# Kernel optimization log

Hardware: AMD Instinct MI355X
Metric: run time of the kernel (lower is better)

## Reference

```python
import jax, jax.numpy as jnp
import numpy as np

B, L, H, NL = 2048, 32, 512, 64  # batch rows, max children, w_dim, num_labels
EPS = 1e-5


def _layernorm(x, g, b):
    mu = jnp.mean(x, axis=-1, keepdims=True)
    var = jnp.mean((x - mu) ** 2, axis=-1, keepdims=True)
    return (x - mu) * jax.lax.rsqrt(var + EPS) * g + b


def _lstm(x, Wih, Whh, bih, bhh):
    # x: [B, L, D] -> h: [B, L, H]; PyTorch gate order i, f, g, o
    Bs, Ls, _ = x.shape
    Hh = Whh.shape[1]
    xg = jnp.einsum('bld,gd->blg', x, Wih) + bih + bhh  # [B, L, 4H]

    def step(carry, xg_t):
        h, c = carry
        gates = xg_t + h @ Whh.T
        i, f, g, o = jnp.split(gates, 4, axis=-1)
        c = jax.nn.sigmoid(f) * c + jax.nn.sigmoid(i) * jnp.tanh(g)
        h = jax.nn.sigmoid(o) * jnp.tanh(c)
        return (h, c), h

    init = (jnp.zeros((Bs, Hh), x.dtype), jnp.zeros((Bs, Hh), x.dtype))
    _, hs = jax.lax.scan(step, init, jnp.swapaxes(xg, 0, 1))
    return jnp.swapaxes(hs, 0, 1)


def setup_inputs() -> dict:
    key = jax.random.key(0)
    ks = jax.random.split(key, 20)
    n = lambda k, shape, s=0.05: (jax.random.normal(k, shape, jnp.float32) * s)
    return {
        'children': n(ks[0], (B, L, H), 1.0),
        'ch_lengths': jax.random.randint(ks[1], (B,), 1, L + 1),
        'nt': n(ks[2], (B, H), 1.0),
        'nt_id': jax.random.randint(ks[3], (B,), 0, NL),
        'stack_state': n(ks[4], (B, H), 1.0),
        'Wih_f': n(ks[5], (4 * H, H)), 'Whh_f': n(ks[6], (4 * H, H)),
        'bih_f': jnp.zeros(4 * H, jnp.float32), 'bhh_f': jnp.zeros(4 * H, jnp.float32),
        'Wih_b': n(ks[7], (4 * H, H)), 'Whh_b': n(ks[8], (4 * H, H)),
        'bih_b': jnp.zeros(4 * H, jnp.float32), 'bhh_b': jnp.zeros(4 * H, jnp.float32),
        'V': n(ks[9], (2 * H, 2 * H)),
        'nt_emb': n(ks[10], (NL, H), 1.0),
        'nt_emb2': n(ks[11], (NL, 2 * H), 1.0),
        'ln1_g': jnp.ones(2 * H, jnp.float32), 'ln1_b': jnp.zeros(2 * H, jnp.float32),
        'ln2_g': jnp.ones(2 * H, jnp.float32), 'ln2_b': jnp.zeros(2 * H, jnp.float32),
        'gate_W': n(ks[12], (2 * H, 4 * H)), 'gate_b': jnp.zeros(2 * H, jnp.float32),
        'out_W': n(ks[13], (H, 2 * H)), 'out_b': jnp.zeros(H, jnp.float32),
    }


def reference(children, ch_lengths, nt, nt_id, stack_state,
              Wih_f, Whh_f, bih_f, bhh_f, Wih_b, Whh_b, bih_b, bhh_b,
              V, nt_emb, nt_emb2, ln1_g, ln1_b, ln2_g, ln2_b,
              gate_W, gate_b, out_W, out_b):
    t = jnp.arange(L)
    valid = (t[None, :] < ch_lengths[:, None])  # [B, L]
    mask = valid[:, :, None].astype(children.dtype)

    # forward direction (padded positions cannot affect earlier outputs)
    h_f = _lstm(children, Wih_f, Whh_f, bih_f, bhh_f) * mask

    # backward direction: emulate packed sequence by per-row reversal over true length
    rev_idx = jnp.clip(ch_lengths[:, None] - 1 - t[None, :], 0, L - 1)  # [B, L]
    x_rev = jnp.take_along_axis(children, rev_idx[:, :, None], axis=1) * mask
    h_b_rev = _lstm(x_rev, Wih_b, Whh_b, bih_b, bhh_b)
    h_b = jnp.take_along_axis(h_b_rev, rev_idx[:, :, None], axis=1) * mask

    h = jnp.concatenate([h_f, h_b], axis=-1)  # [B, L, 2H]

    rhs = jnp.concatenate([nt_emb[nt_id], stack_state], axis=1)  # [B, 2H]
    logit = jnp.einsum('ble,de,bd->bl', h, V, rhs)  # (V h) . rhs
    logit = jnp.where(valid, logit, -jnp.inf)
    attn = jax.nn.softmax(logit, axis=-1)  # [B, L]

    weighted_child = jnp.einsum('ble,bl->be', h, attn)  # [B, 2H]
    weighted_child = _layernorm(weighted_child, ln2_g, ln2_b)

    nt2 = _layernorm(nt_emb2[nt_id], ln1_g, ln1_b)  # [B, 2H]
    gate_in = jnp.concatenate([nt2, weighted_child], axis=-1)  # [B, 4H]
    g = jax.nn.sigmoid(gate_in @ gate_W.T + gate_b)  # [B, 2H]
    c = g * nt2 + (1.0 - g) * weighted_child
    out = jax.nn.relu(c @ out_W.T + out_b)  # [B, H]
    return (out, attn, g)
```

## Files before the change

### kernel.cpp

```cpp
#include <hip/hip_runtime.h>

#define B_ 2048
#define L_ 32
#define H_ 512
#define H2 1024
#define H4 2048

typedef _Float16 half8 __attribute__((ext_vector_type(8)));
typedef _Float16 half4v __attribute__((ext_vector_type(4)));
typedef float f32x4 __attribute__((ext_vector_type(4)));

__device__ __forceinline__ float sigm(float x) { return 1.f / (1.f + __expf(-x)); }
__device__ __forceinline__ float tanh_f(float x) {
  float ax = fabsf(x);
  float e = __expf(2.f * ax);
  float t = 1.f - 2.f / (e + 1.f);
  return x < 0.f ? -t : t;
}
__device__ __forceinline__ float wave_sum(float v) {
#pragma unroll
  for (int o = 32; o; o >>= 1) v += __shfl_xor(v, o);
  return v;
}

__device__ __forceinline__ void gload_lds16(const _Float16* g, _Float16* l) {
  __builtin_amdgcn_global_load_lds((const __attribute__((address_space(1))) void*)g,
                                   (__attribute__((address_space(3))) void*)l, 16, 0, 0);
}

__device__ __forceinline__ void wait_vm8() { asm volatile("s_waitcnt vmcnt(8)" ::: "memory"); }
__device__ __forceinline__ void wait_vm0() { asm volatile("s_waitcnt vmcnt(0)" ::: "memory"); }

__global__ __launch_bounds__(256, 2) void gemm_bt(
    const _Float16* __restrict__ A, int lda,
    const _Float16* __restrict__ Bmat, int ldb,
    float* __restrict__ C, int ldc, int K)
{
  __shared__ _Float16 As[2][128 * 64];
  __shared__ _Float16 Bs[2][128 * 64];
  const int tid = threadIdx.x;
  const int lane = tid & 63;
  const int w = tid >> 6;
  const int n0 = blockIdx.x * 128;
  const int m0 = blockIdx.y * 128;

  const int srow = lane >> 3;
  const int kcs = ((lane & 7) ^ srow) << 3;

  f32x4 acc[4][4] = {};
  const int wm = (w >> 1) * 64;
  const int wn = (w & 1) * 64;
  const int fr = lane & 15;

  const int nkt = K >> 6;
  auto stage = [&](int buf, int kt) {
    const int k0 = kt << 6;
#pragma unroll
    for (int i = 0; i < 4; ++i) {
      const int R0 = w * 32 + i * 8;
      gload_lds16(A + (size_t)(m0 + R0 + srow) * lda + (k0 + kcs), &As[buf][R0 * 64]);
      gload_lds16(Bmat + (size_t)(n0 + R0 + srow) * ldb + (k0 + kcs), &Bs[buf][R0 * 64]);
    }
  };
  auto compute = [&](int buf) {
    const char* Ab = (const char*)&As[buf][0];
    const char* Bb = (const char*)&Bs[buf][0];
#pragma unroll
    for (int kk = 0; kk < 2; ++kk) {
      const int so = (((kk << 2) + (lane >> 4)) ^ (fr & 7)) << 4;
      half8 af[4], bf[4];
#pragma unroll
      for (int m = 0; m < 4; ++m) af[m] = *(const half8*)(Ab + (wm + m * 16 + fr) * 128 + so);
#pragma unroll
      for (int n = 0; n < 4; ++n) bf[n] = *(const half8*)(Bb + (wn + n * 16 + fr) * 128 + so);
#pragma unroll
      for (int m = 0; m < 4; ++m)
#pragma unroll
        for (int n = 0; n < 4; ++n)
          acc[m][n] = __builtin_amdgcn_mfma_f32_16x16x32_f16(af[m], bf[n], acc[m][n], 0, 0, 0);
    }
  };

  stage(0, 0);
  int cur = 0;
  for (int kt = 0; kt < nkt; ++kt) {
    const bool pref = (kt + 1 < nkt);
    if (pref) { stage(cur ^ 1, kt + 1); wait_vm8(); }
    else      { wait_vm0(); }
    __builtin_amdgcn_s_barrier();
    compute(cur);
    __builtin_amdgcn_s_barrier();
    cur ^= 1;
  }

  const int r0 = (lane >> 4) * 4;
#pragma unroll
  for (int m = 0; m < 4; ++m)
#pragma unroll
    for (int n = 0; n < 4; ++n)
#pragma unroll
      for (int r = 0; r < 4; ++r) {
        const int row = m0 + wm + m * 16 + r0 + r;
        const int col = n0 + wn + n * 16 + fr;
        C[(size_t)row * ldc + col] = acc[m][n][r];
      }
}

__global__ __launch_bounds__(256, 2) void gemm_lstm(
    const _Float16* __restrict__ Wpack,
    const float* __restrict__ bpack,
    const _Float16* __restrict__ chH,
    _Float16* __restrict__ hstate,
    float* __restrict__ cstate,
    _Float16* __restrict__ h_all,
    const int* __restrict__ perm,
    const int* __restrict__ lens_sorted,
    int step)
{
  const int lin = blockIdx.x;
  const int xcd = lin & 7;
  const int g8 = lin >> 3;
  const int dir = xcd >> 2;
  const int quad = xcd & 3;
  const int mt = ((g8 >> 3) << 1) + (quad >> 1);
  const int nt = ((quad & 1) << 3) + (g8 & 7);
  const int m0 = mt * 128;
  const int n0 = nt * 128;
  if (lens_sorted[m0] <= step) return;

  __shared__ _Float16 As[2][128 * 64];
  __shared__ _Float16 Bs[2][128 * 64];
  const int tid = threadIdx.x;
  const int lane = tid & 63;
  const int w = tid >> 6;
  const int srow = lane >> 3;
  const int kcs = ((lane & 7) ^ srow) << 3;
  const int wm = (w >> 1) * 64;
  const int wn = (w & 1) * 64;
  const int fr = lane & 15;

  const _Float16* xsrc[4];
  int posr[4];
#pragma unroll
  for (int i = 0; i < 4; ++i) {
    const int pos = m0 + w * 32 + i * 8 + srow;
    const int b = perm[pos];
    int idx;
    if (dir == 0) idx = step;
    else { const int t = lens_sorted[pos] - 1 - step; idx = t < 0 ? 0 : (t > 31 ? 31 : t); }
    xsrc[i] = chH + ((size_t)b * L_ + idx) * H_ + kcs;
    posr[i] = pos;
  }
  const _Float16* Wb = Wpack + (size_t)dir * H4 * H2;
  const _Float16* hprev = hstate + ((size_t)((step & 1) * 2 + dir)) * B_ * H_;
  _Float16* hnext = hstate + ((size_t)(((step + 1) & 1) * 2 + dir)) * B_ * H_;

  f32x4 acc[4][4] = {};

  auto stage = [&](int buf, int kt) {
    const int k0 = kt << 6;
#pragma unroll
    for (int i = 0; i < 4; ++i) {
      const int R0 = w * 32 + i * 8;
      const _Float16* sA = (k0 < 512) ? (xsrc[i] + k0)
                                      : (hprev + (size_t)posr[i] * H_ + (k0 - 512) + kcs);
      gload_lds16(sA, &As[buf][R0 * 64]);
      gload_lds16(Wb + (size_t)(n0 + R0 + srow) * H2 + k0 + kcs, &Bs[buf][R0 * 64]);
    }
  };
  auto compute = [&](int buf) {
    const char* Ab = (const char*)&As[buf][0];
    const char* Bb = (const char*)&Bs[buf][0];
#pragma unroll
    for (int kk = 0; kk < 2; ++kk) {
      const int so = (((kk << 2) + (lane >> 4)) ^ (fr & 7)) << 4;
      half8 af[4], bf[4];
#pragma unroll
      for (int m = 0; m < 4; ++m) af[m] = *(const half8*)(Ab + (wm + m * 16 + fr) * 128 + so);
#pragma unroll
      for (int n = 0; n < 4; ++n) bf[n] = *(const half8*)(Bb + (wn + n * 16 + fr) * 128 + so);
#pragma unroll
      for (int m = 0; m < 4; ++m)
#pragma unroll
        for (int n = 0; n < 4; ++n)
          acc[m][n] = __builtin_amdgcn_mfma_f32_16x16x32_f16(af[m], bf[n], acc[m][n], 0, 0, 0);
    }
  };

  stage(0, 0);
  int cur = 0;
  for (int kt = 0; kt < 16; ++kt) {
    const bool pref = (kt + 1 < 16);
    if (pref) { stage(cur ^ 1, kt + 1); wait_vm8(); }
    else      { wait_vm0(); }
    __builtin_amdgcn_s_barrier();
    compute(cur);
    __builtin_amdgcn_s_barrier();
    cur ^= 1;
  }

  const int r0 = (lane >> 4) * 4;
  const int j = ((n0 + wn) >> 6) * 16 + fr;
  const float bi = bpack[dir * H4 + n0 + wn + 0 * 16 + fr];
  const float bf_ = bpack[dir * H4 + n0 + wn + 1 * 16 + fr];
  const float bg = bpack[dir * H4 + n0 + wn + 2 * 16 + fr];
  const float bo = bpack[dir * H4 + n0 + wn + 3 * 16 + fr];
  float* cs = cstate + (size_t)dir * B_ * H_;

#pragma unroll
  for (int m = 0; m < 4; ++m)
#pragma unroll
    for (int r = 0; r < 4; ++r) {
      const int pos = m0 + wm + m * 16 + r0 + r;
      const float zi = acc[m][0][r] + bi;
      const float zf = acc[m][1][r] + bf_;
      const float zg = acc[m][2][r] + bg;
      const float zo = acc[m][3][r] + bo;
      const size_t ci = (size_t)pos * H_ + j;
      const float cn = sigm(zf) * cs[ci] + sigm(zi) * tanh_f(zg);
      const float h = sigm(zo) * tanh_f(cn);
      cs[ci] = cn;
      hnext[ci] = (_Float16)h;
      const int len = lens_sorted[pos];
      if (step < len) {
        const int b = perm[pos];
        const int t = (dir == 0) ? step : (len - 1 - step);
        h_all[((size_t)b * L_ + t) * H2 + dir * 512 + j] = (_Float16)h;
      }
    }
}

__global__ void cast_half_k(const float* __restrict__ s, _Float16* __restrict__ d, int n) {
  const int i = (blockIdx.x * 256 + threadIdx.x) * 4;
  if (i >= n) return;
  const float4 v = *(const float4*)(s + i);
  half4v h;
  h[0] = (_Float16)v.x; h[1] = (_Float16)v.y; h[2] = (_Float16)v.z; h[3] = (_Float16)v.w;
  *(half4v*)(d + i) = h;
}

__global__ void pack_wcat(const float* __restrict__ Wih_f, const float* __restrict__ Whh_f,
                          const float* __restrict__ Wih_b, const float* __restrict__ Whh_b,
                          _Float16* __restrict__ Wcat) {
  const int idx = blockIdx.x * 256 + threadIdx.x;
  const int k = idx & 511;
  const int c = (idx >> 9) & 2047;
  const int dir = idx >> 20;
  const int g = (c >> 4) & 3;
  const int j = ((c >> 6) << 4) + (c & 15);
  const int n_orig = g * 512 + j;
  const float* Wih = dir ? Wih_b : Wih_f;
  const float* Whh = dir ? Whh_b : Whh_f;
  _Float16* row = Wcat + ((size_t)dir * H4 + c) * H2;
  row[k] = (_Float16)Wih[(size_t)n_orig * H_ + k];
  row[512 + k] = (_Float16)Whh[(size_t)n_orig * H_ + k];
}

__global__ void pack_bias(const float* __restrict__ bih_f, const float* __restrict__ bhh_f,
                          const float* __restrict__ bih_b, const float* __restrict__ bhh_b,
                          float* __restrict__ biascat) {
  const int idx = blockIdx.x * 256 + threadIdx.x;
  const int dir = idx >> 11;
  const int c = idx & 2047;
  const int g = (c >> 4) & 3;
  const int j = ((c >> 6) << 4) + (c & 15);
  const int n = g * 512 + j;
  biascat[idx] = dir ? (bih_b[n] + bhh_b[n]) : (bih_f[n] + bhh_f[n]);
}

__global__ void transpose_v(const float* __restrict__ V, _Float16* __restrict__ Vt) {
  const int idx = blockIdx.x * 256 + threadIdx.x;
  const int d = idx >> 10;
  const int e = idx & 1023;
  Vt[(size_t)e * H2 + d] = (_Float16)V[idx];
}

__global__ void build_rhs(const float* __restrict__ nt_emb, const int* __restrict__ nt_id,
                          const float* __restrict__ stack_state, _Float16* __restrict__ rhs_h) {
  const int idx = blockIdx.x * 256 + threadIdx.x;
  const int b = idx >> 10;
  const int d = idx & 1023;
  const float v = (d < 512) ? nt_emb[(size_t)nt_id[b] * H_ + d]
                            : stack_state[(size_t)b * H_ + (d - 512)];
  rhs_h[idx] = (_Float16)v;
}

__global__ void sort1_k(const int* __restrict__ lens, int* __restrict__ offs, int* __restrict__ cursor) {
  __shared__ int cnt[33];
  const int tid = threadIdx.x;
  if (tid < 33) cnt[tid] = 0;
  __syncthreads();
  for (int i = tid; i < B_; i += 256) atomicAdd(&cnt[lens[i]], 1);
  __syncthreads();
  if (tid == 0) {
    int acc = 0;
    for (int l = 32; l >= 1; --l) { offs[l] = acc; acc += cnt[l]; }
  }
  if (tid < 33) cursor[tid] = 0;
}

__global__ void sort2_k(const int* __restrict__ lens, const int* __restrict__ offs,
                        int* __restrict__ cursor, int* __restrict__ perm,
                        int* __restrict__ lens_sorted) {
  const int b = blockIdx.x * 256 + threadIdx.x;
  const int len = lens[b];
  const int pos = offs[len] + atomicAdd(&cursor[len], 1);
  perm[pos] = b;
  lens_sorted[pos] = len;
}

__global__ void marker_k(float* out) { out[threadIdx.x] = 12345.0f; }

__global__ __launch_bounds__(256) void attn_kernel(
    const _Float16* __restrict__ h_all, const float* __restrict__ u,
    const int* __restrict__ lens,
    const float* __restrict__ g2, const float* __restrict__ b2,
    float* __restrict__ attn_out, float* __restrict__ wc_f, _Float16* __restrict__ gin_h) {
  __shared__ float u_s[H2];
  __shared__ float logit_s[L_];
  __shared__ float attn_s[L_];
  __shared__ float red_s[8];
  const int b = blockIdx.x;
  const int tid = threadIdx.x;
  const int lane = tid & 63;
  const int w = tid >> 6;
#pragma unroll
  for (int r = 0; r < 4; ++r) u_s[tid + r * 256] = u[(size_t)b * H2 + tid + r * 256];
  __syncthreads();
  const _Float16* hb = h_all + (size_t)b * L_ * H2;
  const int len = lens[b];
#pragma unroll
  for (int li = 0; li < 8; ++li) {
    const int l = w * 8 + li;
    float p = 0.f;
    if (l < len) {
      const _Float16* hr = hb + (size_t)l * H2;
#pragma unroll
      for (int j = 0; j < 16; ++j) {
        const int e = lane + 64 * j;
        p += (float)hr[e] * u_s[e];
      }
      p = wave_sum(p);
    }
    if (lane == 0) logit_s[l] = p;
  }
  __syncthreads();
  if (w == 0) {
    const int l = lane;
    float v = (l < len) ? logit_s[l] : -1e30f;
    float m = v;
#pragma unroll
    for (int o = 32; o; o >>= 1) m = fmaxf(m, __shfl_xor(m, o));
    const float e = (l < len) ? __expf(v - m) : 0.f;
    float s = e;
#pragma unroll
    for (int o = 32; o; o >>= 1) s += __shfl_xor(s, o);
    const float a = e / s;
    if (l < L_) { attn_s[l] = a; attn_out[(size_t)b * L_ + l] = a; }
  }
  __syncthreads();
  float wcv[4] = {0.f, 0.f, 0.f, 0.f};
  for (int l = 0; l < len; ++l) {
    const float a = attn_s[l];
    const _Float16* hr = hb + (size_t)l * H2;
#pragma unroll
    for (int r = 0; r < 4; ++r) wcv[r] += a * (float)hr[tid + r * 256];
  }
  float s1 = wcv[0] + wcv[1] + wcv[2] + wcv[3];
  float s2 = wcv[0] * wcv[0] + wcv[1] * wcv[1] + wcv[2] * wcv[2] + wcv[3] * wcv[3];
  s1 = wave_sum(s1);
  s2 = wave_sum(s2);
  if (lane == 0) { red_s[w] = s1; red_s[4 + w] = s2; }
  __syncthreads();
  const float S1 = red_s[0] + red_s[1] + red_s[2] + red_s[3];
  const float S2 = red_s[4] + red_s[5] + red_s[6] + red_s[7];
  const float mu = S1 * (1.f / H2);
  const float var = S2 * (1.f / H2) - mu * mu;
  const float rstd = rsqrtf(var + 1e-5f);
#pragma unroll
  for (int r = 0; r < 4; ++r) {
    const int e = tid + r * 256;
    const float y = (wcv[r] - mu) * rstd * g2[e] + b2[e];
    wc_f[(size_t)b * H2 + e] = y;
    gin_h[(size_t)b * H4 + H2 + e] = (_Float16)y;
  }
}

__global__ __launch_bounds__(256) void nt2_kernel(
    const float* __restrict__ nt_emb2, const int* __restrict__ nt_id,
    const float* __restrict__ g1, const float* __restrict__ b1,
    float* __restrict__ nt2_f, _Float16* __restrict__ gin_h) {
  __shared__ float red_s[8];
  const int b = blockIdx.x;
  const int tid = threadIdx.x;
  const int lane = tid & 63;
  const int w = tid >> 6;
  const float* x = nt_emb2 + (size_t)nt_id[b] * H2;
  float v[4];
  float s1 = 0.f, s2 = 0.f;
#pragma unroll
  for (int r = 0; r < 4; ++r) {
    v[r] = x[tid + r * 256];
    s1 += v[r];
    s2 += v[r] * v[r];
  }
  s1 = wave_sum(s1);
  s2 = wave_sum(s2);
  if (lane == 0) { red_s[w] = s1; red_s[4 + w] = s2; }
  __syncthreads();
  const float S1 = red_s[0] + red_s[1] + red_s[2] + red_s[3];
  const float S2 = red_s[4] + red_s[5] + red_s[6] + red_s[7];
  const float mu = S1 * (1.f / H2);
  const float var = S2 * (1.f / H2) - mu * mu;
  const float rstd = rsqrtf(var + 1e-5f);
#pragma unroll
  for (int r = 0; r < 4; ++r) {
    const int e = tid + r * 256;
    const float y = (v[r] - mu) * rstd * g1[e] + b1[e];
    nt2_f[(size_t)b * H2 + e] = y;
    gin_h[(size_t)b * H4 + e] = (_Float16)y;
  }
}

__global__ void gate_epi(const float* __restrict__ gpre, const float* __restrict__ gate_b,
                         const float* __restrict__ nt2_f, const float* __restrict__ wc_f,
                         float* __restrict__ g_out, _Float16* __restrict__ cmix_h) {
  const int idx = blockIdx.x * 256 + threadIdx.x;
  const int j = idx & (H2 - 1);
  const float g = sigm(gpre[idx] + gate_b[j]);
  g_out[idx] = g;
  const float c = g * nt2_f[idx] + (1.f - g) * wc_f[idx];
  cmix_h[idx] = (_Float16)c;
}

__global__ void out_epi(const float* __restrict__ opre, const float* __restrict__ out_b,
                        float* __restrict__ outp) {
  const int idx = blockIdx.x * 256 + threadIdx.x;
  const int j = idx & (H_ - 1);
  const float v = opre[idx] + out_b[j];
  outp[idx] = v > 0.f ? v : 0.f;
}

extern "C" void kernel_launch(void* const* d_in, const int* in_sizes, int n_in,
                              void* d_out, int out_size, void* d_ws, size_t ws_size,
                              hipStream_t stream) {
  const float* children = (const float*)d_in[0];
  const int* lens = (const int*)d_in[1];
  const int* nt_id = (const int*)d_in[3];
  const float* stack_state = (const float*)d_in[4];
  const float* Wih_f = (const float*)d_in[5];
  const float* Whh_f = (const float*)d_in[6];
  const float* bih_f = (const float*)d_in[7];
  const float* bhh_f = (const float*)d_in[8];
  const float* Wih_b = (const float*)d_in[9];
  const float* Whh_b = (const float*)d_in[10];
  const float* bih_b = (const float*)d_in[11];
  const float* bhh_b = (const float*)d_in[12];
  const float* V = (const float*)d_in[13];
  const float* nt_emb = (const float*)d_in[14];
  const float* nt_emb2 = (const float*)d_in[15];
  const float* ln1_g = (const float*)d_in[16];
  const float* ln1_b = (const float*)d_in[17];
  const float* ln2_g = (const float*)d_in[18];
  const float* ln2_b = (const float*)d_in[19];
  const float* gate_W = (const float*)d_in[20];
  const float* gate_b = (const float*)d_in[21];
  const float* out_W = (const float*)d_in[22];
  const float* out_b = (const float*)d_in[23];

  float* out = (float*)d_out;
  float* attn_out = out + (size_t)B_ * H_;
  float* g_out = attn_out + (size_t)B_ * L_;

  char* wsp = (char*)d_ws;
  size_t off = 0;
  auto alloc = [&](size_t bytes) {
    char* p = wsp + off;
    off += (bytes + 255) & ~(size_t)255;
    return p;
  };
  _Float16* ch_h = (_Float16*)alloc((size_t)B_ * L_ * H_ * 2);
  _Float16* h_all = (_Float16*)alloc((size_t)B_ * L_ * H2 * 2);
  _Float16* Wcat = (_Float16*)alloc((size_t)2 * H4 * H2 * 2);
  float* biascat = (float*)alloc((size_t)2 * H4 * 4);
  _Float16* Vt = (_Float16*)alloc((size_t)H2 * H2 * 2);
  _Float16* gateWh = (_Float16*)alloc((size_t)H2 * H4 * 2);
  _Float16* outWh = (_Float16*)alloc((size_t)H_ * H2 * 2);
  _Float16* rhs_h = (_Float16*)alloc((size_t)B_ * H2 * 2);
  float* u_f = (float*)alloc((size_t)B_ * H2 * 4);
  _Float16* hstate = (_Float16*)alloc((size_t)2 * 2 * B_ * H_ * 2);
  float* cstate = (float*)alloc((size_t)2 * B_ * H_ * 4);
  float* wc_f = (float*)alloc((size_t)B_ * H2 * 4);
  float* nt2_f = (float*)alloc((size_t)B_ * H2 * 4);
  _Float16* gin_h = (_Float16*)alloc((size_t)B_ * H4 * 2);
  float* gpre_f = (float*)alloc((size_t)B_ * H2 * 4);
  _Float16* cmix_h = (_Float16*)alloc((size_t)B_ * H2 * 2);
  float* opre_f = (float*)alloc((size_t)B_ * H_ * 4);
  int* sort_offs = (int*)alloc(64 * 4);
  int* sort_cursor = (int*)alloc(64 * 4);
  int* perm = (int*)alloc((size_t)B_ * 4);
  int* lens_sorted = (int*)alloc((size_t)B_ * 4);

  if (off > ws_size) {
    marker_k<<<1, 64, 0, stream>>>(out);
    return;
  }

  cast_half_k<<<32768, 256, 0, stream>>>(children, ch_h, B_ * L_ * H_);
  cast_half_k<<<2048, 256, 0, stream>>>(gate_W, gateWh, H2 * H4);
  cast_half_k<<<512, 256, 0, stream>>>(out_W, outWh, H_ * H2);
  pack_wcat<<<8192, 256, 0, stream>>>(Wih_f, Whh_f, Wih_b, Whh_b, Wcat);
  pack_bias<<<16, 256, 0, stream>>>(bih_f, bhh_f, bih_b, bhh_b, biascat);
  transpose_v<<<4096, 256, 0, stream>>>(V, Vt);
  build_rhs<<<8192, 256, 0, stream>>>(nt_emb, nt_id, stack_state, rhs_h);
  hipMemsetAsync(hstate, 0, (size_t)2 * 2 * B_ * H_ * 2, stream);
  hipMemsetAsync(cstate, 0, (size_t)2 * B_ * H_ * 4, stream);
  sort1_k<<<1, 256, 0, stream>>>(lens, sort_offs, sort_cursor);
  sort2_k<<<8, 256, 0, stream>>>(lens, sort_offs, sort_cursor, perm, lens_sorted);
  nt2_kernel<<<2048, 256, 0, stream>>>(nt_emb2, nt_id, ln1_g, ln1_b, nt2_f, gin_h);

  gemm_bt<<<dim3(8, 16, 1), 256, 0, stream>>>(rhs_h, H2, Vt, H2, u_f, H2, H2);

  for (int t = 0; t < 32; ++t) {
    gemm_lstm<<<512, 256, 0, stream>>>(
        Wcat, biascat, ch_h, hstate, cstate, h_all, perm, lens_sorted, t);
  }

  attn_kernel<<<2048, 256, 0, stream>>>(h_all, u_f, lens, ln2_g, ln2_b, attn_out, wc_f, gin_h);

  gemm_bt<<<dim3(8, 16, 1), 256, 0, stream>>>(gin_h, H4, gateWh, H4, gpre_f, H2, H4);
  gate_epi<<<8192, 256, 0, stream>>>(gpre_f, gate_b, nt2_f, wc_f, g_out, cmix_h);

  gemm_bt<<<dim3(4, 16, 1), 256, 0, stream>>>(cmix_h, H2, outWh, H2, opre_f, H_, H2);
  out_epi<<<4096, 256, 0, stream>>>(opre_f, out_b, out);
}
```

Measured before the change: 1.092 ms.

## Load LSTM weight fragments directly into registers instead of staging through LDS

In the per-step LSTM gate kernel, the weight (B) tiles are now read from global memory straight into registers in MFMA fragment layout, double-buffered across even and odd k-tiles. Only the activation (A) tiles still go through LDS via async global-to-LDS loads, with the wait thresholds adjusted to the new count of outstanding loads. This removes the B shared-memory buffer and its LDS reads, which halves LDS use and may allow more resident blocks. The cost is more registers and uncoalesced 16-byte global reads of weights, each lane fetching its own row segment.

```diff
diff --git a/kernel.cpp b/kernel.cpp
--- a/kernel.cpp
+++ b/kernel.cpp
@@ -28,8 +28,9 @@
                                    (__attribute__((address_space(3))) void*)l, 16, 0, 0);
 }
 
-__device__ __forceinline__ void wait_vm8() { asm volatile("s_waitcnt vmcnt(8)" ::: "memory"); }
-__device__ __forceinline__ void wait_vm0() { asm volatile("s_waitcnt vmcnt(0)" ::: "memory"); }
+__device__ __forceinline__ void wait_vm12() { asm volatile("s_waitcnt vmcnt(12)" ::: "memory"); }
+__device__ __forceinline__ void wait_vm8()  { asm volatile("s_waitcnt vmcnt(8)"  ::: "memory"); }
+__device__ __forceinline__ void wait_vm0()  { asm volatile("s_waitcnt vmcnt(0)"  ::: "memory"); }
 
 __global__ __launch_bounds__(256, 2) void gemm_bt(
     const _Float16* __restrict__ A, int lda,
@@ -129,7 +130,6 @@
   if (lens_sorted[m0] <= step) return;
 
   __shared__ _Float16 As[2][128 * 64];
-  __shared__ _Float16 Bs[2][128 * 64];
   const int tid = threadIdx.x;
   const int lane = tid & 63;
   const int w = tid >> 6;
@@ -138,6 +138,7 @@
   const int wm = (w >> 1) * 64;
   const int wn = (w & 1) * 64;
   const int fr = lane & 15;
+  const int fk = (lane >> 4) * 8;
 
   const _Float16* xsrc[4];
   int posr[4];
@@ -155,9 +156,14 @@
   const _Float16* hprev = hstate + ((size_t)((step & 1) * 2 + dir)) * B_ * H_;
   _Float16* hnext = hstate + ((size_t)(((step + 1) & 1) * 2 + dir)) * B_ * H_;
 
+  const _Float16* wrow[4];
+#pragma unroll
+  for (int n = 0; n < 4; ++n)
+    wrow[n] = Wb + (size_t)(n0 + wn + n * 16 + fr) * H2 + fk;
+
   f32x4 acc[4][4] = {};
 
-  auto stage = [&](int buf, int kt) {
+  auto stageA = [&](int buf, int kt) {
     const int k0 = kt << 6;
 #pragma unroll
     for (int i = 0; i < 4; ++i) {
@@ -165,38 +171,54 @@
       const _Float16* sA = (k0 < 512) ? (xsrc[i] + k0)
                                       : (hprev + (size_t)posr[i] * H_ + (k0 - 512) + kcs);
       gload_lds16(sA, &As[buf][R0 * 64]);
-      gload_lds16(Wb + (size_t)(n0 + R0 + srow) * H2 + k0 + kcs, &Bs[buf][R0 * 64]);
     }
   };
-  auto compute = [&](int buf) {
+  auto loadB = [&](half8 (&bf)[4][2], int kt) {
+#pragma unroll
+    for (int n = 0; n < 4; ++n)
+#pragma unroll
+      for (int kk = 0; kk < 2; ++kk)
+        bf[n][kk] = *(const half8*)(wrow[n] + kt * 64 + kk * 32);
+  };
+  auto computeK = [&](int buf, half8 (&bf)[4][2]) {
     const char* Ab = (const char*)&As[buf][0];
-    const char* Bb = (const char*)&Bs[buf][0];
 #pragma unroll
     for (int kk = 0; kk < 2; ++kk) {
       const int so = (((kk << 2) + (lane >> 4)) ^ (fr & 7)) << 4;
-      half8 af[4], bf[4];
+      half8 af[4];
 #pragma unroll
       for (int m = 0; m < 4; ++m) af[m] = *(const half8*)(Ab + (wm + m * 16 + fr) * 128 + so);
 #pragma unroll
-      for (int n = 0; n < 4; ++n) bf[n] = *(const half8*)(Bb + (wn + n * 16 + fr) * 128 + so);
-#pragma unroll
       for (int m = 0; m < 4; ++m)
 #pragma unroll
         for (int n = 0; n < 4; ++n)
-          acc[m][n] = __builtin_amdgcn_mfma_f32_16x16x32_f16(af[m], bf[n], acc[m][n], 0, 0, 0);
+          acc[m][n] = __builtin_amdgcn_mfma_f32_16x16x32_f16(af[m], bf[n][kk], acc[m][n], 0, 0, 0);
     }
   };
 
-  stage(0, 0);
-  int cur = 0;
-  for (int kt = 0; kt < 16; ++kt) {
-    const bool pref = (kt + 1 < 16);
-    if (pref) { stage(cur ^ 1, kt + 1); wait_vm8(); }
-    else      { wait_vm0(); }
+  half8 bEven[4][2], bOdd[4][2];
+  stageA(0, 0);
+  loadB(bEven, 0);
+
+#pragma unroll 1
+  for (int kt = 0; kt < 16; kt += 2) {
+    stageA(1, kt + 1);
+    loadB(bOdd, kt + 1);
+    wait_vm12();
     __builtin_amdgcn_s_barrier();
-    compute(cur);
+    computeK(0, bEven);
     __builtin_amdgcn_s_barrier();
-    cur ^= 1;
+
+    if (kt + 2 < 16) {
+      stageA(0, kt + 2);
+      loadB(bEven, kt + 2);
+      wait_vm12();
+    } else {
+      wait_vm0();
+    }
+    __builtin_amdgcn_s_barrier();
+    computeK(1, bOdd);
+    __builtin_amdgcn_s_barrier();
   }
 
   const int r0 = (lane >> 4) * 4;
```

After: 1.464 ms. +34.1%, slower.
